# Optimization experiments

Measured on AMD Instinct MI355X. Metric: run time of the kernel, lower is better.

## Reference

```python
import jax, jax.numpy as jnp
import numpy as np

N_NODES = 50000
N_EDGES = 1600000
IN_CH = 512
HID = 8      # per-head features, layer 1
HEADS = 8
OUT_CH = 40  # num classes
NEG_SLOPE = 0.2  # PyG GATConv default leaky_relu slope


def setup_inputs() -> dict:
    key = jax.random.key(0)
    ks = jax.random.split(key, 8)
    x = jax.random.uniform(ks[0], (N_NODES, IN_CH), dtype=jnp.float32)
    edge_index = jax.random.randint(ks[1], (2, N_EDGES), 0, N_NODES, dtype=jnp.int64)
    s1 = 1.0 / np.sqrt(IN_CH)
    s2 = 1.0 / np.sqrt(HEADS * HID)
    W1 = jax.random.normal(ks[2], (IN_CH, HEADS * HID), dtype=jnp.float32) * s1
    att_src1 = jax.random.normal(ks[3], (HEADS, HID), dtype=jnp.float32) * s2
    att_dst1 = jax.random.normal(ks[4], (HEADS, HID), dtype=jnp.float32) * s2
    b1 = jnp.zeros((HEADS * HID,), dtype=jnp.float32)
    W2 = jax.random.normal(ks[5], (HEADS * HID, OUT_CH), dtype=jnp.float32) * s2
    att_src2 = jax.random.normal(ks[6], (1, OUT_CH), dtype=jnp.float32) * 0.15
    att_dst2 = jax.random.normal(ks[7], (1, OUT_CH), dtype=jnp.float32) * 0.15
    b2 = jnp.zeros((OUT_CH,), dtype=jnp.float32)
    return {"x": x, "edge_index": edge_index, "W1": W1, "att_src1": att_src1,
            "att_dst1": att_dst1, "b1": b1, "W2": W2, "att_src2": att_src2,
            "att_dst2": att_dst2, "b2": b2}


def _row_normalize(x):
    return x / jnp.clip(x.sum(axis=1, keepdims=True), 1e-8, None)


def _gat_conv(x, src, dst, W, att_src, att_dst, bias, heads, out_ch, concat):
    """PyG GATConv (self-loops already included in src/dst)."""
    n = x.shape[0]
    h = (x @ W).reshape(n, heads, out_ch)          # [N, H, C]
    a_src = jnp.sum(h * att_src, axis=-1)          # [N, H]
    a_dst = jnp.sum(h * att_dst, axis=-1)          # [N, H]
    alpha = jax.nn.leaky_relu(a_src[src] + a_dst[dst], NEG_SLOPE)  # [E, H]
    # segment softmax over incoming edges of each dst node
    m = jax.ops.segment_max(alpha, dst, num_segments=n)            # [N, H]
    e = jnp.exp(alpha - m[dst])
    denom = jax.ops.segment_sum(e, dst, num_segments=n)            # [N, H]
    alpha = e / (denom[dst] + 1e-16)
    msg = h[src] * alpha[:, :, None]               # [E, H, C]
    out = jax.ops.segment_sum(msg, dst, num_segments=n)            # [N, H, C]
    out = out.reshape(n, heads * out_ch) if concat else out.mean(axis=1)
    return out + bias


def reference(x, edge_index, W1, att_src1, att_dst1, b1, W2, att_src2, att_dst2, b2):
    n = x.shape[0]
    loops = jnp.arange(n, dtype=edge_index.dtype)
    src = jnp.concatenate([edge_index[0], loops])
    dst = jnp.concatenate([edge_index[1], loops])
    h = _row_normalize(x)
    # dropout omitted: inference mode (training=False)
    h = jax.nn.elu(_gat_conv(h, src, dst, W1, att_src1, att_dst1, b1, HEADS, HID, True))
    return _gat_conv(h, src, dst, W2, att_src2, att_dst2, b2, 1, OUT_CH, False)
```

## Files before the change

### kernel.cpp

```cpp
#include <hip/hip_runtime.h>
#include <math.h>

#define N_NODES 50000
#define IN_CH   512
#define HID     8
#define HEADS   8
#define C1      64
#define OUT_CH  40
#define NEG_SLOPE 0.2f
#define NB      ((N_NODES + 255) / 256)
#define TILE    4096
#define CAP     16384

__device__ __forceinline__ float leaky(float v) { return fmaxf(v, NEG_SLOPE * v); }
__device__ __forceinline__ float fexp(float v) { return __expf(v); }

typedef __attribute__((ext_vector_type(8))) short short8;
typedef __attribute__((ext_vector_type(4))) short short4v;
typedef __attribute__((ext_vector_type(4))) float f32x4;

__device__ __forceinline__ unsigned short f2bf(float f) {
    unsigned u = __builtin_bit_cast(unsigned, f);
    u += 0x7FFFu + ((u >> 16) & 1u);
    return (unsigned short)(u >> 16);
}
__device__ __forceinline__ float bf2f(unsigned short h) {
    unsigned u = ((unsigned)h) << 16;
    return __builtin_bit_cast(float, u);
}

#define XH_STRIDE_B 272

__global__ __launch_bounds__(256) void k_packW(
    const float* __restrict__ W1, short* __restrict__ bph, short* __restrict__ bpl,
    int* __restrict__ coarseCur)
{
    const int idx = blockIdx.x * 256 + threadIdx.x;
    if (blockIdx.x == 0 && threadIdx.x < NB)
        coarseCur[threadIdx.x] = threadIdx.x * CAP;
    if (idx >= 512 * 64) return;
    const int k = idx >> 6, col = idx & 63;
    const float w = W1[idx];
    const unsigned short hi = f2bf(w);
    const unsigned short lo = f2bf(w - bf2f(hi));
    const int di = ((k >> 5) * 64 + col) * 32 + (k & 31);
    bph[di] = (short)hi;
    bpl[di] = (short)lo;
}

__global__ __launch_bounds__(256) void k_gemm1_mfma(
    const float* __restrict__ x,
    const short* __restrict__ bph, const short* __restrict__ bpl,
    const float* __restrict__ attS, const float* __restrict__ attD,
    unsigned short* __restrict__ h1b, float* __restrict__ aS, float* __restrict__ aD)
{
    __shared__ unsigned char smem[17536];
    short* xh = (short*)smem;
    short* xl = (short*)(smem + 8704);
    float* rowsum = (float*)(smem + 17408);
    float* houtf  = (float*)smem;

    const int tid  = threadIdx.x;
    const int lane = tid & 63;
    const int w    = tid >> 6;
    const int row_off = (w & 1) * 16;
    const int col_off = (w >> 1) * 32;
    const int rowBase = blockIdx.x * 32;

    const int l15 = lane & 15;
    const int kg  = lane >> 4;
    const int a_base = (l15 + row_off) * XH_STRIDE_B + kg * 16;

    const int srow = tid >> 5;
    const int sk4  = tid & 31;

    f32x4 acc0 = {0.f, 0.f, 0.f, 0.f};
    f32x4 acc1 = {0.f, 0.f, 0.f, 0.f};
    float psum[4] = {0.f, 0.f, 0.f, 0.f};
    float4 va[4], vb[4];

    auto LOAD = [&](int c, float4 (&v)[4]) {
        #pragma unroll
        for (int i = 0; i < 4; ++i) {
            const int grow = rowBase + i * 8 + srow;
            v[i] = (grow < N_NODES)
                 ? *(const float4*)(x + (size_t)grow * IN_CH + c * 128 + sk4 * 4)
                 : make_float4(0.f, 0.f, 0.f, 0.f);
        }
    };
    auto STAGE = [&](float4 (&v)[4]) {
        #pragma unroll
        for (int i = 0; i < 4; ++i) {
            const int row = i * 8 + srow;
            const unsigned short h0 = f2bf(v[i].x), h1u = f2bf(v[i].y),
                                 h2 = f2bf(v[i].z), h3  = f2bf(v[i].w);
            short4v hvv = { (short)h0, (short)h1u, (short)h2, (short)h3 };
            short4v lvv = { (short)f2bf(v[i].x - bf2f(h0)), (short)f2bf(v[i].y - bf2f(h1u)),
                            (short)f2bf(v[i].z - bf2f(h2)), (short)f2bf(v[i].w - bf2f(h3)) };
            *(short4v*)((char*)xh + row * XH_STRIDE_B + sk4 * 8) = hvv;
            *(short4v*)((char*)xl + row * XH_STRIDE_B + sk4 * 8) = lvv;
            psum[i] += v[i].x + v[i].y + v[i].z + v[i].w;
        }
    };
    auto MFMA = [&](int c) {
        #pragma unroll
        for (int kk2 = 0; kk2 < 4; ++kk2) {
            const int kk = c * 4 + kk2;
            const short8 ah = *(const short8*)((const char*)xh + a_base + kk2 * 64);
            const short8 al = *(const short8*)((const char*)xl + a_base + kk2 * 64);
            const int b0 = (kk * 64 + col_off + l15) * 32 + kg * 8;
            const int b1 = b0 + 16 * 32;
            const short8 bh0 = *(const short8*)(bph + b0);
            const short8 bl0 = *(const short8*)(bpl + b0);
            const short8 bh1 = *(const short8*)(bph + b1);
            const short8 bl1 = *(const short8*)(bpl + b1);
            acc0 = __builtin_amdgcn_mfma_f32_16x16x32_bf16(ah, bh0, acc0, 0, 0, 0);
            acc1 = __builtin_amdgcn_mfma_f32_16x16x32_bf16(ah, bh1, acc1, 0, 0, 0);
            acc0 = __builtin_amdgcn_mfma_f32_16x16x32_bf16(ah, bl0, acc0, 0, 0, 0);
            acc1 = __builtin_amdgcn_mfma_f32_16x16x32_bf16(ah, bl1, acc1, 0, 0, 0);
            acc0 = __builtin_amdgcn_mfma_f32_16x16x32_bf16(al, bh0, acc0, 0, 0, 0);
            acc1 = __builtin_amdgcn_mfma_f32_16x16x32_bf16(al, bh1, acc1, 0, 0, 0);
        }
    };

    LOAD(0, va);
    STAGE(va);
    __syncthreads();
    LOAD(1, vb);
    MFMA(0);
    __syncthreads();
    STAGE(vb);
    __syncthreads();
    LOAD(2, va);
    MFMA(1);
    __syncthreads();
    STAGE(va);
    __syncthreads();
    LOAD(3, vb);
    MFMA(2);
    __syncthreads();
    STAGE(vb);
    #pragma unroll
    for (int i = 0; i < 4; ++i) {
        float s = psum[i];
        #pragma unroll
        for (int off = 16; off; off >>= 1) s += __shfl_xor(s, off, 32);
        if (sk4 == 0) rowsum[i * 8 + srow] = s;
    }
    __syncthreads();
    MFMA(3);
    __syncthreads();

    #pragma unroll
    for (int r = 0; r < 4; ++r) {
        const int row = row_off + kg * 4 + r;
        const float rs = fmaxf(rowsum[row], 1e-8f);
        houtf[row * 68 + col_off + l15]      = acc0[r] / rs;
        houtf[row * 68 + col_off + 16 + l15] = acc1[r] / rs;
    }
    __syncthreads();

    #pragma unroll
    for (int i = tid; i < 32 * 16; i += 256) {
        const int row = i >> 4, seg = i & 15;
        if (rowBase + row < N_NODES) {
            const float* hs = houtf + row * 68 + seg * 4;
            short4v o = { (short)f2bf(hs[0]), (short)f2bf(hs[1]),
                          (short)f2bf(hs[2]), (short)f2bf(hs[3]) };
            *(short4v*)(h1b + (size_t)(rowBase + row) * 64 + seg * 4) = o;
        }
    }

    {
        const int row = tid >> 3, hd = tid & 7;
        if (rowBase + row < N_NODES) {
            float vs = 0.f, vd = 0.f;
            #pragma unroll
            for (int e2 = 0; e2 < 8; ++e2) {
                const float hv = houtf[row * 68 + hd * 8 + e2];
                vs = fmaf(hv, attS[hd * 8 + e2], vs);
                vd = fmaf(hv, attD[hd * 8 + e2], vd);
            }
            aS[(size_t)(rowBase + row) * 8 + hd] = vs;
            aD[(size_t)(rowBase + row) * 8 + hd] = vd;
        }
    }
}

__global__ __launch_bounds__(256) void k_part(
    const int* __restrict__ src, const int* __restrict__ dst, int E,
    int* __restrict__ coarseCur, unsigned int* __restrict__ pairs)
{
    __shared__ int  hist[256];
    __shared__ int  scn[256];
    __shared__ int  offs[256];
    __shared__ unsigned int  pairBuf[TILE];
    __shared__ unsigned char bktBuf[TILE];

    const int t = threadIdx.x;
    const int tileBase = blockIdx.x * TILE;
    const int n = min(TILE, E - tileBase);

    hist[t] = 0;
    __syncthreads();

    for (int e = t; e < n; e += 256)
        atomicAdd(&hist[dst[tileBase + e] >> 8], 1);
    __syncthreads();

    scn[t] = hist[t];
    __syncthreads();
    #pragma unroll
    for (int off = 1; off < 256; off <<= 1) {
        int xv = (t >= off) ? scn[t - off] : 0;
        __syncthreads();
        scn[t] += xv;
        __syncthreads();
    }

    {
        const int h  = hist[t];
        const int ls = scn[t] - h;
        int off = 0;
        if (h > 0) {
            const int gbase = atomicAdd(&coarseCur[t], h);
            off = gbase - ls;
        }
        offs[t] = off;
        hist[t] = ls;
    }
    __syncthreads();

    for (int e = t; e < n; e += 256) {
        const int s = src[tileBase + e];
        const int d = dst[tileBase + e];
        const int bkt = d >> 8;
        const int pos = atomicAdd(&hist[bkt], 1);
        pairBuf[pos] = (unsigned)s | ((unsigned)(d & 255) << 17);
        bktBuf[pos]  = (unsigned char)bkt;
    }
    __syncthreads();

    for (int i = t; i < n; i += 256)
        pairs[i + offs[bktBuf[i]]] = pairBuf[i];
}

__global__ __launch_bounds__(256) void k_fine2(
    const int* __restrict__ coarseCur,
    const unsigned int* __restrict__ pairs, int* __restrict__ ssrc,
    int* __restrict__ cumS, int* __restrict__ cumE)
{
    __shared__ int hist[256];
    __shared__ int scn[256];
    __shared__ int cur[256];
    const int b = blockIdx.x;
    const int t = threadIdx.x;
    const int dbase = b << 8;
    const int nd = min(256, N_NODES - dbase);
    const int lo = b * CAP;
    const int hi = coarseCur[b];

    hist[t] = 0;
    __syncthreads();
    for (int j = lo + t; j < hi; j += 256)
        atomicAdd(&hist[(pairs[j] >> 17) & 255], 1);
    __syncthreads();

    const int hv = hist[t];
    scn[t] = hv;
    __syncthreads();
    #pragma unroll
    for (int off = 1; off < 256; off <<= 1) {
        int xv = (t >= off) ? scn[t - off] : 0;
        __syncthreads();
        scn[t] += xv;
        __syncthreads();
    }
    if (t < nd) {
        cumS[dbase + t] = lo + scn[t] - hv;
        cumE[dbase + t] = lo + scn[t];
    }
    cur[t] = lo + scn[t] - hv;
    __syncthreads();

    for (int j = lo + t; j < hi; j += 256) {
        const unsigned int p = pairs[j];
        const int pos = atomicAdd(&cur[(p >> 17) & 255], 1);
        ssrc[pos] = (int)(p & 0x1FFFFu);
    }
}

__global__ __launch_bounds__(256) void k_agg1f(
    const int* __restrict__ cumS, const int* __restrict__ cumE,
    const int* __restrict__ ssrc,
    const float* __restrict__ aS, const float* __restrict__ aD,
    const unsigned short* __restrict__ h1b, const float* __restrict__ b1,
    const float* __restrict__ W2,
    const float* __restrict__ attS2, const float* __restrict__ attD2,
    unsigned short* __restrict__ h2b, float* __restrict__ a2s, float* __restrict__ a2d)
{
    __shared__ float w2s[64 * 40];
    __shared__ float hstage[4][64];

    const int tid  = threadIdx.x;
    const int lane = tid & 63;
    const int w    = tid >> 6;
    const int node = __builtin_amdgcn_readfirstlane(blockIdx.x * 4 + w);
    const int e = lane >> 3;
    const int c = lane & 7;

    #pragma unroll
    for (int i = tid; i < 640; i += 256)
        ((float4*)w2s)[i] = ((const float4*)W2)[i];

    const int start = cumS[node];
    const int end   = cumE[node];

    const float aDn = aD[(size_t)node * 8 + c];
    float acc[8] = {0.f, 0.f, 0.f, 0.f, 0.f, 0.f, 0.f, 0.f};
    float den = 0.f;

    if (e == 0) {
        const float e0 = fexp(leaky(aS[(size_t)node * 8 + c] + aDn));
        const short8 hv = *(const short8*)(h1b + (size_t)node * 64 + c * 8);
        #pragma unroll
        for (int j = 0; j < 8; ++j)
            acc[j] = e0 * bf2f((unsigned short)hv[j]);
        den = e0;
    }

    int base = start;
    for (; base + 32 <= end; base += 32) {
        const int s0 = ssrc[base + e];
        const int s1 = ssrc[base + 8 + e];
        const int s2 = ssrc[base + 16 + e];
        const int s3 = ssrc[base + 24 + e];
        const float aa0 = aS[(size_t)s0 * 8 + c];
        const float aa1 = aS[(size_t)s1 * 8 + c];
        const float aa2 = aS[(size_t)s2 * 8 + c];
        const float aa3 = aS[(size_t)s3 * 8 + c];
        const short8 h0 = *(const short8*)(h1b + ((size_t)s0 << 6) + c * 8);
        const short8 h1v = *(const short8*)(h1b + ((size_t)s1 << 6) + c * 8);
        const short8 h2v = *(const short8*)(h1b + ((size_t)s2 << 6) + c * 8);
        const short8 h3v = *(const short8*)(h1b + ((size_t)s3 << 6) + c * 8);
        const float w0 = fexp(leaky(aa0 + aDn));
        const float w1 = fexp(leaky(aa1 + aDn));
        const float w2 = fexp(leaky(aa2 + aDn));
        const float w3 = fexp(leaky(aa3 + aDn));
        #pragma unroll
        for (int j = 0; j < 8; ++j) {
            acc[j] = fmaf(w0, bf2f((unsigned short)h0[j]), acc[j]);
            acc[j] = fmaf(w1, bf2f((unsigned short)h1v[j]), acc[j]);
            acc[j] = fmaf(w2, bf2f((unsigned short)h2v[j]), acc[j]);
            acc[j] = fmaf(w3, bf2f((unsigned short)h3v[j]), acc[j]);
        }
        den += w0 + w1 + w2 + w3;
    }
    for (; base + 8 <= end; base += 8) {
        const int s = ssrc[base + e];
        const float aa = aS[(size_t)s * 8 + c];
        const short8 hv = *(const short8*)(h1b + ((size_t)s << 6) + c * 8);
        const float wv = fexp(leaky(aa + aDn));
        #pragma unroll
        for (int j = 0; j < 8; ++j)
            acc[j] = fmaf(wv, bf2f((unsigned short)hv[j]), acc[j]);
        den += wv;
    }
    if (base < end) {
        const int nb  = end - base;
        const int idx = base + (e < nb ? e : nb - 1);
        const int s   = ssrc[idx];
        float wv = fexp(leaky(aS[(size_t)s * 8 + c] + aDn));
        if (e >= nb) wv = 0.f;
        const short8 hv = *(const short8*)(h1b + ((size_t)s << 6) + c * 8);
        #pragma unroll
        for (int j = 0; j < 8; ++j)
            acc[j] = fmaf(wv, bf2f((unsigned short)hv[j]), acc[j]);
        den += wv;
    }

    #pragma unroll
    for (int m = 8; m < 64; m <<= 1) {
        den += __shfl_xor(den, m, 64);
        #pragma unroll
        for (int j = 0; j < 8; ++j)
            acc[j] += __shfl_xor(acc[j], m, 64);
    }

    if (e == 0) {
        const float dinv = 1.f / (den + 1e-16f);
        #pragma unroll
        for (int j = 0; j < 8; ++j) {
            const float v = acc[j] * dinv + b1[c * 8 + j];
            hstage[w][c * 8 + j] = v > 0.f ? v : (__expf(v) - 1.f);
        }
    }
    __syncthreads();

    const int j = lane;
    float acc2 = 0.f;
    if (j < OUT_CH) {
        #pragma unroll
        for (int k = 0; k < 64; ++k)
            acc2 = fmaf(hstage[w][k], w2s[k * 40 + j], acc2);
    }
    float vs = (j < OUT_CH) ? acc2 * attS2[j] : 0.f;
    float vd = (j < OUT_CH) ? acc2 * attD2[j] : 0.f;
    #pragma unroll
    for (int off = 32; off; off >>= 1) {
        vs += __shfl_xor(vs, off, 64);
        vd += __shfl_xor(vd, off, 64);
    }
    if (j < OUT_CH) h2b[(size_t)node * 40 + j] = f2bf(acc2);
    if (j == 0) {
        a2s[node] = vs;
        a2d[node] = vd;
    }
}

__global__ __launch_bounds__(256) void k_agg2(
    const int* __restrict__ cumS, const int* __restrict__ cumE,
    const int* __restrict__ ssrc,
    const float* __restrict__ a2s, const float* __restrict__ a2d,
    const unsigned short* __restrict__ h2b, const float* __restrict__ b2,
    float* __restrict__ out)
{
    const int lane = threadIdx.x & 63;
    const int node = __builtin_amdgcn_readfirstlane(blockIdx.x * 4 + (threadIdx.x >> 6));
    const int e = lane >> 3;
    const int c = lane & 7;

    const int start = cumS[node];
    const int end   = cumE[node];

    const float aDd = a2d[node];
    float acc[8] = {0.f, 0.f, 0.f, 0.f, 0.f, 0.f, 0.f, 0.f};
    float den = 0.f;

    if (e == 0) {
        const float e0 = fexp(leaky(a2s[node] + aDd));
        const short8 hv = *(const short8*)(h2b + (size_t)node * 40 + c * 8);
        #pragma unroll
        for (int j = 0; j < 8; ++j)
            acc[j] = e0 * bf2f((unsigned short)hv[j]);
        den = e0;
    }

    int base = start;
    for (; base + 32 <= end; base += 32) {
        const int s0 = ssrc[base + e];
        const int s1 = ssrc[base + 8 + e];
        const int s2 = ssrc[base + 16 + e];
        const int s3 = ssrc[base + 24 + e];
        const float aa0 = a2s[s0];
        const float aa1 = a2s[s1];
        const float aa2 = a2s[s2];
        const float aa3 = a2s[s3];
        const short8 h0 = *(const short8*)(h2b + (size_t)s0 * 40 + c * 8);
        const short8 h1v = *(const short8*)(h2b + (size_t)s1 * 40 + c * 8);
        const short8 h2v = *(const short8*)(h2b + (size_t)s2 * 40 + c * 8);
        const short8 h3v = *(const short8*)(h2b + (size_t)s3 * 40 + c * 8);
        const float w0 = fexp(leaky(aa0 + aDd));
        const float w1 = fexp(leaky(aa1 + aDd));
        const float w2 = fexp(leaky(aa2 + aDd));
        const float w3 = fexp(leaky(aa3 + aDd));
        #pragma unroll
        for (int j = 0; j < 8; ++j) {
            acc[j] = fmaf(w0, bf2f((unsigned short)h0[j]), acc[j]);
            acc[j] = fmaf(w1, bf2f((unsigned short)h1v[j]), acc[j]);
            acc[j] = fmaf(w2, bf2f((unsigned short)h2v[j]), acc[j]);
            acc[j] = fmaf(w3, bf2f((unsigned short)h3v[j]), acc[j]);
        }
        den += w0 + w1 + w2 + w3;
    }
    for (; base + 8 <= end; base += 8) {
        const int s = ssrc[base + e];
        const float aa = a2s[s];
        const short8 hv = *(const short8*)(h2b + (size_t)s * 40 + c * 8);
        const float wv = fexp(leaky(aa + aDd));
        #pragma unroll
        for (int j = 0; j < 8; ++j)
            acc[j] = fmaf(wv, bf2f((unsigned short)hv[j]), acc[j]);
        den += wv;
    }
    if (base < end) {
        const int nb  = end - base;
        const int idx = base + (e < nb ? e : nb - 1);
        const int s   = ssrc[idx];
        float wv = fexp(leaky(a2s[s] + aDd));
        if (e >= nb) wv = 0.f;
        const short8 hv = *(const short8*)(h2b + (size_t)s * 40 + c * 8);
        #pragma unroll
        for (int j = 0; j < 8; ++j)
            acc[j] = fmaf(wv, bf2f((unsigned short)hv[j]), acc[j]);
        den += wv;
    }

    #pragma unroll
    for (int m = 8; m < 64; m <<= 1) {
        den += __shfl_xor(den, m, 64);
        #pragma unroll
        for (int j = 0; j < 8; ++j)
            acc[j] += __shfl_xor(acc[j], m, 64);
    }

    if (e == 0 && c < 5) {
        const float dinv = 1.f / (den + 1e-16f);
        float o[8];
        #pragma unroll
        for (int j = 0; j < 8; ++j)
            o[j] = acc[j] * dinv + b2[c * 8 + j];
        float4* dst0 = (float4*)(out + (size_t)node * OUT_CH + c * 8);
        dst0[0] = make_float4(o[0], o[1], o[2], o[3]);
        dst0[1] = make_float4(o[4], o[5], o[6], o[7]);
    }
}

extern "C" void kernel_launch(void* const* d_in, const int* in_sizes, int n_in,
                              void* d_out, int out_size, void* d_ws, size_t ws_size,
                              hipStream_t stream)
{
    const float* x     = (const float*)d_in[0];
    const int*   ei    = (const int*)d_in[1];
    const float* W1    = (const float*)d_in[2];
    const float* attS1 = (const float*)d_in[3];
    const float* attD1 = (const float*)d_in[4];
    const float* b1    = (const float*)d_in[5];
    const float* W2    = (const float*)d_in[6];
    const float* attS2 = (const float*)d_in[7];
    const float* attD2 = (const float*)d_in[8];
    const float* b2    = (const float*)d_in[9];

    const int E = in_sizes[1] / 2;
    const int* src = ei;
    const int* dst = ei + E;

    float* out = (float*)d_out;
    float* f = (float*)d_ws;
    float* aS1  = f;  f += (size_t)N_NODES * 8;
    float* aD1  = f;  f += (size_t)N_NODES * 8;
    float* a2s  = f;  f += (size_t)N_NODES;
    float* a2d  = f;  f += (size_t)N_NODES;
    unsigned short* h1b = (unsigned short*)f;  f += (size_t)N_NODES * 32;
    unsigned short* h2b = (unsigned short*)f;  f += (size_t)N_NODES * 20 + 64;
    short* bph = (short*)f;  f += 16384;
    short* bpl = (short*)f;  f += 16384;
    unsigned int* pairs = (unsigned int*)f;  f += (size_t)NB * CAP;
    int* ip = (int*)f;
    int* coarseCur = ip;  ip += 256;
    int* cumS      = ip;  ip += N_NODES;
    int* cumE      = ip;  ip += N_NODES;
    int* ssrc      = ip;  ip += (size_t)NB * CAP;

    const int partBlocks = (E + TILE - 1) / TILE;

    k_packW<<<(512 * 64 + 255) / 256, 256, 0, stream>>>(W1, bph, bpl, coarseCur);

    k_part<<<partBlocks, 256, 0, stream>>>(src, dst, E, coarseCur, pairs);
    k_fine2<<<NB, 256, 0, stream>>>(coarseCur, pairs, ssrc, cumS, cumE);

    k_gemm1_mfma<<<(N_NODES + 31) / 32, 256, 0, stream>>>(x, bph, bpl, attS1, attD1,
                                                          h1b, aS1, aD1);
    k_agg1f<<<N_NODES / 4, 256, 0, stream>>>(cumS, cumE, ssrc, aS1, aD1, h1b, b1,
                                             W2, attS2, attD2, h2b, a2s, a2d);

    k_agg2<<<N_NODES / 4, 256, 0, stream>>>(cumS, cumE, ssrc, a2s, a2d, h2b, b2, out);
}
```

Baseline: 177.9 us.

## Merge independent preprocessing kernels into shared launches via block-index dispatch

The weight-packing and edge-partition kernels are merged into one launch, and the fine-sort kernel runs in the same launch as the layer-1 GEMM, with blocks picking their role by block index. coarseCur now holds relative counts, zeroed by a memset, and bucket bases are added explicitly. This cuts kernel launches and lets independent work overlap on the GPU, at the cost of an extra memset and mixed block types that can hurt occupancy and shared-memory sizing.

Result: faster. 171.3 us (-3.7%).

```diff
diff --git a/kernel.cpp b/kernel.cpp
--- a/kernel.cpp
+++ b/kernel.cpp
@@ -11,6 +11,8 @@
 #define NB      ((N_NODES + 255) / 256)
 #define TILE    4096
 #define CAP     16384
+#define PACKW_BLOCKS 128
+#define GEMM1_BLOCKS ((N_NODES + 31) / 32)
 
 __device__ __forceinline__ float leaky(float v) { return fmaxf(v, NEG_SLOPE * v); }
 __device__ __forceinline__ float fexp(float v) { return __expf(v); }
@@ -31,36 +33,137 @@
 
 #define XH_STRIDE_B 272
 
-__global__ __launch_bounds__(256) void k_packW(
+__global__ __launch_bounds__(256) void k_pre(
     const float* __restrict__ W1, short* __restrict__ bph, short* __restrict__ bpl,
-    int* __restrict__ coarseCur)
+    const int* __restrict__ src, const int* __restrict__ dst, int E,
+    int* __restrict__ coarseCur, unsigned int* __restrict__ pairs)
 {
-    const int idx = blockIdx.x * 256 + threadIdx.x;
-    if (blockIdx.x == 0 && threadIdx.x < NB)
-        coarseCur[threadIdx.x] = threadIdx.x * CAP;
-    if (idx >= 512 * 64) return;
-    const int k = idx >> 6, col = idx & 63;
-    const float w = W1[idx];
-    const unsigned short hi = f2bf(w);
-    const unsigned short lo = f2bf(w - bf2f(hi));
-    const int di = ((k >> 5) * 64 + col) * 32 + (k & 31);
-    bph[di] = (short)hi;
-    bpl[di] = (short)lo;
-}
-
-__global__ __launch_bounds__(256) void k_gemm1_mfma(
+    __shared__ int  hist[256];
+    __shared__ int  scn[256];
+    __shared__ int  offs[256];
+    __shared__ unsigned int  pairBuf[TILE];
+    __shared__ unsigned char bktBuf[TILE];
+
+    const int t = threadIdx.x;
+
+    if (blockIdx.x < PACKW_BLOCKS) {
+        const int idx = blockIdx.x * 256 + t;
+        const int k = idx >> 6, col = idx & 63;
+        const float w = W1[idx];
+        const unsigned short hi = f2bf(w);
+        const unsigned short lo = f2bf(w - bf2f(hi));
+        const int di = ((k >> 5) * 64 + col) * 32 + (k & 31);
+        bph[di] = (short)hi;
+        bpl[di] = (short)lo;
+        return;
+    }
+
+    const int tileBase = (blockIdx.x - PACKW_BLOCKS) * TILE;
+    const int n = min(TILE, E - tileBase);
+
+    hist[t] = 0;
+    __syncthreads();
+
+    for (int e = t; e < n; e += 256)
+        atomicAdd(&hist[dst[tileBase + e] >> 8], 1);
+    __syncthreads();
+
+    scn[t] = hist[t];
+    __syncthreads();
+    #pragma unroll
+    for (int off = 1; off < 256; off <<= 1) {
+        int xv = (t >= off) ? scn[t - off] : 0;
+        __syncthreads();
+        scn[t] += xv;
+        __syncthreads();
+    }
+
+    {
+        const int h  = hist[t];
+        const int ls = scn[t] - h;
+        int off = 0;
+        if (h > 0) {
+            const int gbase = t * CAP + atomicAdd(&coarseCur[t], h);
+            off = gbase - ls;
+        }
+        offs[t] = off;
+        hist[t] = ls;
+    }
+    __syncthreads();
+
+    for (int e = t; e < n; e += 256) {
+        const int s = src[tileBase + e];
+        const int d = dst[tileBase + e];
+        const int bkt = d >> 8;
+        const int pos = atomicAdd(&hist[bkt], 1);
+        pairBuf[pos] = (unsigned)s | ((unsigned)(d & 255) << 17);
+        bktBuf[pos]  = (unsigned char)bkt;
+    }
+    __syncthreads();
+
+    for (int i = t; i < n; i += 256)
+        pairs[i + offs[bktBuf[i]]] = pairBuf[i];
+}
+
+__global__ __launch_bounds__(256) void k_mid(
     const float* __restrict__ x,
     const short* __restrict__ bph, const short* __restrict__ bpl,
     const float* __restrict__ attS, const float* __restrict__ attD,
-    unsigned short* __restrict__ h1b, float* __restrict__ aS, float* __restrict__ aD)
+    unsigned short* __restrict__ h1b, float* __restrict__ aS, float* __restrict__ aD,
+    const int* __restrict__ coarseCur, const unsigned int* __restrict__ pairs,
+    int* __restrict__ ssrc, int* __restrict__ cumS, int* __restrict__ cumE)
 {
     __shared__ unsigned char smem[17536];
+
+    const int tid = threadIdx.x;
+
+    if (blockIdx.x >= GEMM1_BLOCKS) {
+        int* hist = (int*)smem;
+        int* scn  = hist + 256;
+        int* cur  = scn + 256;
+        const int b = blockIdx.x - GEMM1_BLOCKS;
+        const int t = tid;
+        const int dbase = b << 8;
+        const int nd = min(256, N_NODES - dbase);
+        const int lo = b * CAP;
+        const int hi = lo + coarseCur[b];
+
+        hist[t] = 0;
+        __syncthreads();
+        for (int j = lo + t; j < hi; j += 256)
+            atomicAdd(&hist[(pairs[j] >> 17) & 255], 1);
+        __syncthreads();
+
+        const int hv = hist[t];
+        scn[t] = hv;
+        __syncthreads();
+        #pragma unroll
+        for (int off = 1; off < 256; off <<= 1) {
+            int xv = (t >= off) ? scn[t - off] : 0;
+            __syncthreads();
+            scn[t] += xv;
+            __syncthreads();
+        }
+        if (t < nd) {
+            cumS[dbase + t] = lo + scn[t] - hv;
+            cumE[dbase + t] = lo + scn[t];
+        }
+        cur[t] = lo + scn[t] - hv;
+        __syncthreads();
+
+        for (int j = lo + t; j < hi; j += 256) {
+            const unsigned int p = pairs[j];
+            const int pos = atomicAdd(&cur[(p >> 17) & 255], 1);
+            ssrc[pos] = (int)(p & 0x1FFFFu);
+        }
+        return;
+    }
+
     short* xh = (short*)smem;
     short* xl = (short*)(smem + 8704);
     float* rowsum = (float*)(smem + 17408);
     float* houtf  = (float*)smem;
 
-    const int tid  = threadIdx.x;
     const int lane = tid & 63;
     const int w    = tid >> 6;
     const int row_off = (w & 1) * 16;
@@ -184,109 +287,6 @@
             aS[(size_t)(rowBase + row) * 8 + hd] = vs;
             aD[(size_t)(rowBase + row) * 8 + hd] = vd;
         }
-    }
-}
-
-__global__ __launch_bounds__(256) void k_part(
-    const int* __restrict__ src, const int* __restrict__ dst, int E,
-    int* __restrict__ coarseCur, unsigned int* __restrict__ pairs)
-{
-    __shared__ int  hist[256];
-    __shared__ int  scn[256];
-    __shared__ int  offs[256];
-    __shared__ unsigned int  pairBuf[TILE];
-    __shared__ unsigned char bktBuf[TILE];
-
-    const int t = threadIdx.x;
-    const int tileBase = blockIdx.x * TILE;
-    const int n = min(TILE, E - tileBase);
-
-    hist[t] = 0;
-    __syncthreads();
-
-    for (int e = t; e < n; e += 256)
-        atomicAdd(&hist[dst[tileBase + e] >> 8], 1);
-    __syncthreads();
-
-    scn[t] = hist[t];
-    __syncthreads();
-    #pragma unroll
-    for (int off = 1; off < 256; off <<= 1) {
-        int xv = (t >= off) ? scn[t - off] : 0;
-        __syncthreads();
-        scn[t] += xv;
-        __syncthreads();
-    }
-
-    {
-        const int h  = hist[t];
-        const int ls = scn[t] - h;
-        int off = 0;
-        if (h > 0) {
-            const int gbase = atomicAdd(&coarseCur[t], h);
-            off = gbase - ls;
-        }
-        offs[t] = off;
-        hist[t] = ls;
-    }
-    __syncthreads();
-
-    for (int e = t; e < n; e += 256) {
-        const int s = src[tileBase + e];
-        const int d = dst[tileBase + e];
-        const int bkt = d >> 8;
-        const int pos = atomicAdd(&hist[bkt], 1);
-        pairBuf[pos] = (unsigned)s | ((unsigned)(d & 255) << 17);
-        bktBuf[pos]  = (unsigned char)bkt;
-    }
-    __syncthreads();
-
-    for (int i = t; i < n; i += 256)
-        pairs[i + offs[bktBuf[i]]] = pairBuf[i];
-}
-
-__global__ __launch_bounds__(256) void k_fine2(
-    const int* __restrict__ coarseCur,
-    const unsigned int* __restrict__ pairs, int* __restrict__ ssrc,
-    int* __restrict__ cumS, int* __restrict__ cumE)
-{
-    __shared__ int hist[256];
-    __shared__ int scn[256];
-    __shared__ int cur[256];
-    const int b = blockIdx.x;
-    const int t = threadIdx.x;
-    const int dbase = b << 8;
-    const int nd = min(256, N_NODES - dbase);
-    const int lo = b * CAP;
-    const int hi = coarseCur[b];
-
-    hist[t] = 0;
-    __syncthreads();
-    for (int j = lo + t; j < hi; j += 256)
-        atomicAdd(&hist[(pairs[j] >> 17) & 255], 1);
-    __syncthreads();
-
-    const int hv = hist[t];
-    scn[t] = hv;
-    __syncthreads();
-    #pragma unroll
-    for (int off = 1; off < 256; off <<= 1) {
-        int xv = (t >= off) ? scn[t - off] : 0;
-        __syncthreads();
-        scn[t] += xv;
-        __syncthreads();
-    }
-    if (t < nd) {
-        cumS[dbase + t] = lo + scn[t] - hv;
-        cumE[dbase + t] = lo + scn[t];
-    }
-    cur[t] = lo + scn[t] - hv;
-    __syncthreads();
-
-    for (int j = lo + t; j < hi; j += 256) {
-        const unsigned int p = pairs[j];
-        const int pos = atomicAdd(&cur[(p >> 17) & 255], 1);
-        ssrc[pos] = (int)(p & 0x1FFFFu);
     }
 }
 
@@ -554,13 +554,15 @@
 
     const int partBlocks = (E + TILE - 1) / TILE;
 
-    k_packW<<<(512 * 64 + 255) / 256, 256, 0, stream>>>(W1, bph, bpl, coarseCur);
-
-    k_part<<<partBlocks, 256, 0, stream>>>(src, dst, E, coarseCur, pairs);
-    k_fine2<<<NB, 256, 0, stream>>>(coarseCur, pairs, ssrc, cumS, cumE);
-
-    k_gemm1_mfma<<<(N_NODES + 31) / 32, 256, 0, stream>>>(x, bph, bpl, attS1, attD1,
-                                                          h1b, aS1, aD1);
+    hipMemsetAsync(coarseCur, 0, 256 * sizeof(int), stream);
+
+    k_pre<<<PACKW_BLOCKS + partBlocks, 256, 0, stream>>>(W1, bph, bpl,
+                                                         src, dst, E, coarseCur, pairs);
+
+    k_mid<<<GEMM1_BLOCKS + NB, 256, 0, stream>>>(x, bph, bpl, attS1, attD1,
+                                                 h1b, aS1, aD1,
+                                                 coarseCur, pairs, ssrc, cumS, cumE);
+
     k_agg1f<<<N_NODES / 4, 256, 0, stream>>>(cumS, cumE, ssrc, aS1, aD1, h1b, b1,
                                              W2, attS2, attD2, h2b, a2s, a2d);
 
```
